# Kernel optimization log

Measured on AMD Instinct MI355X. Metric: run time of the kernel, lower is better.

Reference implementation:

```python
import jax, jax.numpy as jnp
import numpy as np

S, B, K = 1024, 16, 1024
QD, KD = 1024, 1024


def setup_inputs() -> dict:
    key = jax.random.key(0)
    k1, k2, k3, k4 = jax.random.split(key, 4)
    queries = jax.random.normal(k1, (S, B, QD), dtype=jnp.float32)
    keys = jax.random.normal(k2, (B, K, KD), dtype=jnp.float32)
    null_mask = jax.random.randint(k3, (B, K), 0, 2).astype(jnp.bool_)
    W_in = jax.random.normal(k4, (KD, QD), dtype=jnp.float32) * 0.02
    return {"queries": queries, "keys": keys, "null_mask": null_mask, "W_in": W_in}


def reference(queries, keys, null_mask, W_in):
    # queries: (S, B, QD); keys: (B, K, KD); null_mask: (B, K); W_in: (KD, QD)
    t_query = jnp.einsum('sbq,dq->sbd', queries, W_in)          # linear_in, no bias
    alpha = jnp.einsum('sbd,bkd->sbk', t_query, keys)           # unscaled bilinear scores
    alpha = jnp.where(null_mask[None, :, :], -jnp.inf, alpha)   # masked_fill_
    att_weight = jax.nn.softmax(alpha, axis=2)                  # (S, B, K)
    attened_keys = jnp.einsum('sbk,bkd->sbd', att_weight, keys) # (S, B, KD)
    return (attened_keys, alpha)
```

## Files before the change

kernel.cpp:

```cpp
#include <hip/hip_runtime.h>
#include <math.h>

#define S_DIM 1024
#define B_DIM 16
#define K_DIM 1024
#define QD_DIM 1024
#define KD_DIM 1024
#define MASK_NEG (-3.0e38f)

using short8v = __attribute__((ext_vector_type(8))) short;
using float4v = __attribute__((ext_vector_type(4))) float;
using uint4v  = __attribute__((ext_vector_type(4))) uint;

#define MFMA(a, b, c) __builtin_amdgcn_mfma_f32_16x16x32_bf16(a, b, c, 0, 0, 0)
#define BAR()   __builtin_amdgcn_s_barrier()
#define SB0()   __builtin_amdgcn_sched_barrier(0)
#define PRIO(x) __builtin_amdgcn_s_setprio(x)
#define VMCNT(N) asm volatile("s_waitcnt vmcnt(" #N ")" ::: "memory")
#define LGKM0()  asm volatile("s_waitcnt lgkmcnt(0)" ::: "memory")


__device__ __forceinline__ void gll16(const void* g, void* l) {
    __builtin_amdgcn_global_load_lds((const __attribute__((address_space(1))) unsigned int*)g,
                                     (__attribute__((address_space(3))) unsigned int*)l,
                                     16, 0, 0);
}

__device__ __forceinline__ void split4(const float4 v, uint2& hi, uint2& lo) {
    uint ax = __float_as_uint(v.x), ay = __float_as_uint(v.y);
    uint az = __float_as_uint(v.z), aw = __float_as_uint(v.w);
    hi.x = __builtin_amdgcn_perm(ay, ax, 0x07060302u);
    hi.y = __builtin_amdgcn_perm(aw, az, 0x07060302u);
    float rx = v.x - __uint_as_float(ax & 0xFFFF0000u);
    float ry = v.y - __uint_as_float(ay & 0xFFFF0000u);
    float rz = v.z - __uint_as_float(az & 0xFFFF0000u);
    float rw = v.w - __uint_as_float(aw & 0xFFFF0000u);
    lo.x = __builtin_amdgcn_perm(__float_as_uint(ry), __float_as_uint(rx), 0x07060302u);
    lo.y = __builtin_amdgcn_perm(__float_as_uint(rw), __float_as_uint(rz), 0x07060302u);
}

__device__ __forceinline__ int twiddle(int l) {
    int b0 = (l ^ (l >> 2) ^ (l >> 4)) & 1;
    int b1 = ((l >> 1) ^ (l >> 3)) & 1;
    int b2 = ((l >> 2) ^ (l >> 4)) & 1;
    return (l & 0x38) | (b2 << 2) | (b1 << 1) | b0;
}
__device__ __forceinline__ int fragoff(int R, int quad) {
    return (((R << 2) | quad) ^ (R & 7)) << 3;
}

struct Ctx {
    int w, quad, l15, wm, wn, srow, scol;
    int arow, ac, ws0, ws1;
    int offA[4], offB[8];
};

__device__ __forceinline__ Ctx make_ctx(int t) {
    Ctx c;
    const int lane = t & 63;
    c.w = t >> 6; c.quad = lane >> 4; c.l15 = lane & 15;
    c.wm = c.w >> 1; c.wn = c.w & 1;
    const int sl = twiddle(lane);
    c.srow = c.w * 32 + (sl >> 2);
    c.scol = (sl & 3) * 8;
    c.arow = t >> 1; c.ac = t & 1;
    const int c0 = c.ac * 2;
    c.ws0 = ((c.arow << 2) | c0) ^ (c.arow & 7);
    c.ws1 = ((c.arow << 2) | (c0 + 1)) ^ (c.arow & 7);
    #pragma unroll
    for (int mt = 0; mt < 4; ++mt) { int R = c.wm * 64 + mt * 16 + c.l15; c.offA[mt] = fragoff(R, c.quad); }
    #pragma unroll
    for (int nt = 0; nt < 8; ++nt) { int R = c.wn * 128 + nt * 16 + c.l15; c.offB[nt] = fragoff(R, c.quad); }
    return c;
}

__device__ __forceinline__ void stage2(const short* __restrict__ plane, int row0, int k0,
                                       short* tile, const Ctx& c) {
    const short* g0 = plane + (size_t)(row0 + c.srow) * 1024 + k0 + c.scol;
    gll16(g0, tile + c.w * 1024);
    gll16(g0 + (size_t)16 * 1024, tile + c.w * 1024 + 512);
}

__device__ __forceinline__ void mfma8x4(const short8v (&a)[4], const short8v (&bb)[8],
                                        float4v (&acc)[4][8]) {
    #pragma unroll
    for (int nt = 0; nt < 8; ++nt)
        #pragma unroll
        for (int mt = 0; mt < 4; ++mt)
            acc[mt][nt] = MFMA(a[mt], bb[nt], acc[mt][nt]);
}

__device__ __forceinline__ void load4(const float4* __restrict__ P, int kn, float4 (&v)[4]) {
    #pragma unroll
    for (int i = 0; i < 4; ++i) v[i] = P[kn / 4 + i];
}

__device__ __forceinline__ void write_split(const float4 (&va)[4], short* N0, short* N1,
                                            int ws0, int ws1) {
    uint2 h[4], l[4];
    #pragma unroll
    for (int i = 0; i < 4; ++i) split4(va[i], h[i], l[i]);
    uint4v v0, v1;
    v0[0] = h[0].x; v0[1] = h[0].y; v0[2] = h[1].x; v0[3] = h[1].y;
    v1[0] = h[2].x; v1[1] = h[2].y; v1[2] = h[3].x; v1[3] = h[3].y;
    *(uint4v*)(N0 + ws0 * 8) = v0;
    *(uint4v*)(N0 + ws1 * 8) = v1;
    v0[0] = l[0].x; v0[1] = l[0].y; v0[2] = l[1].x; v0[3] = l[1].y;
    v1[0] = l[2].x; v1[1] = l[2].y; v1[2] = l[3].x; v1[3] = l[3].y;
    *(uint4v*)(N1 + ws0 * 8) = v0;
    *(uint4v*)(N1 + ws1 * 8) = v1;
}

__device__ __forceinline__ void writeA_exp(const float4 (&va)[4], float Mv, float Lv,
                                           short* N0, short* N1, int ws0, int ws1) {
    float4 p[4];
    #pragma unroll
    for (int i = 0; i < 4; ++i) {
        p[i].x = __expf(va[i].x - Mv) * Lv;
        p[i].y = __expf(va[i].y - Mv) * Lv;
        p[i].z = __expf(va[i].z - Mv) * Lv;
        p[i].w = __expf(va[i].w - Mv) * Lv;
    }
    write_split(p, N0, N1, ws0, ws1);
}

__global__ __launch_bounds__(256) void k_split(const float* __restrict__ src,
                                               short* __restrict__ h, short* __restrict__ l) {
    const size_t base = ((size_t)blockIdx.x * 256 + threadIdx.x) * 4;
    const float4 v = *(const float4*)(src + base);
    uint2 hh, ll;
    split4(v, hh, ll);
    *(uint2*)(h + base) = hh;
    *(uint2*)(l + base) = ll;
}

__global__ __launch_bounds__(256) void k_transpose(const float* __restrict__ keys,
                                                   short* __restrict__ th, short* __restrict__ tl) {
    __shared__ float T[32][33];
    const int t = threadIdx.x;
    const int b = blockIdx.z, d0 = blockIdx.x * 32, k0 = blockIdx.y * 32;
    const float* Kb = keys + (size_t)b * K_DIM * KD_DIM;
    const int ry = t >> 3, cx = (t & 7) * 4;
    const float4 v = *(const float4*)(Kb + (size_t)(k0 + ry) * KD_DIM + d0 + cx);
    T[ry][cx] = v.x; T[ry][cx + 1] = v.y; T[ry][cx + 2] = v.z; T[ry][cx + 3] = v.w;
    __syncthreads();
    float4 g;
    g.x = T[cx][ry]; g.y = T[cx + 1][ry]; g.z = T[cx + 2][ry]; g.w = T[cx + 3][ry];
    uint2 hh, ll;
    split4(g, hh, ll);
    const size_t o = (size_t)b * K_DIM * KD_DIM + (size_t)(d0 + ry) * K_DIM + k0 + cx;
    *(uint2*)(th + o) = hh;
    *(uint2*)(tl + o) = ll;
}

__global__ __launch_bounds__(256) void k_stats(const float* __restrict__ alpha,
                                               float* __restrict__ mx,
                                               float* __restrict__ il) {
    const int r = blockIdx.x;
    const int t = threadIdx.x;
    const float4 v = ((const float4*)(alpha + (size_t)r * K_DIM))[t];
    float m = fmaxf(fmaxf(v.x, v.y), fmaxf(v.z, v.w));
    #pragma unroll
    for (int o = 1; o < 64; o <<= 1) m = fmaxf(m, __shfl_xor(m, o, 64));
    __shared__ float redm[4];
    __shared__ float reds[4];
    const int wid = t >> 6;
    if ((t & 63) == 0) redm[wid] = m;
    __syncthreads();
    const float M = fmaxf(fmaxf(redm[0], redm[1]), fmaxf(redm[2], redm[3]));
    float s = expf(v.x - M) + expf(v.y - M) + expf(v.z - M) + expf(v.w - M);
    #pragma unroll
    for (int o = 1; o < 64; o <<= 1) s += __shfl_xor(s, o, 64);
    if ((t & 63) == 0) reds[wid] = s;
    __syncthreads();
    if (t == 0) {
        mx[r] = M;
        il[r] = 1.0f / (reds[0] + reds[1] + reds[2] + reds[3]);
    }
}

template<bool DS>
__device__ __forceinline__ void step_g1(const float4* __restrict__ qP, int kn,
                                        const short* __restrict__ Wh, const short* __restrict__ Wl, int n0,
                                        const short* C0, const short* C1, const short* C2, const short* C3,
                                        short* N0, short* N1, short* N2, short* N3,
                                        const Ctx& c, float4v (&acc)[4][8]) {
    short8v ah[4], bh[8];
    #pragma unroll
    for (int mt = 0; mt < 4; ++mt) ah[mt] = *(const short8v*)(C0 + c.offA[mt]);
    #pragma unroll
    for (int nt = 0; nt < 8; ++nt) bh[nt] = *(const short8v*)(C2 + c.offB[nt]);
    float4 qv[4];
    if (DS) { load4(qP, kn, qv); SB0(); stage2(Wh, n0, kn, N2, c); }
    SB0(); BAR(); LGKM0(); SB0();
    PRIO(1); mfma8x4(ah, bh, acc); PRIO(0); SB0(); BAR();

    short8v al[4];
    #pragma unroll
    for (int mt = 0; mt < 4; ++mt) al[mt] = *(const short8v*)(C1 + c.offA[mt]);
    if (DS) { stage2(Wl, n0, kn, N3, c); }
    SB0(); BAR(); LGKM0(); SB0();
    PRIO(1); mfma8x4(al, bh, acc); PRIO(0); SB0(); BAR();

    if (DS) { VMCNT(4); } else { VMCNT(0); }
    SB0(); BAR();
    short8v bl[8];
    #pragma unroll
    for (int nt = 0; nt < 8; ++nt) bl[nt] = *(const short8v*)(C3 + c.offB[nt]);
    LGKM0(); SB0();
    PRIO(1); mfma8x4(ah, bl, acc); PRIO(0);
    if (DS) {
        write_split(qv, N0, N1, c.ws0, c.ws1);
        LGKM0();
        VMCNT(2);
    }
    SB0(); BAR();
}

__global__ __launch_bounds__(512, 2) void g1k(const float* __restrict__ Q,
                                              const short* __restrict__ Wh, const short* __restrict__ Wl,
                                              short* __restrict__ TQh, short* __restrict__ TQl) {
    __shared__ __align__(16) short lds[65536];
    const int t = threadIdx.x;
    const int m0 = blockIdx.y * 256, n0 = blockIdx.x * 256;
    const Ctx c = make_ctx(t);
    const float4* qP = (const float4*)(Q + (size_t)(m0 + c.arow) * QD_DIM + c.ac * 16);
    short *T00 = lds,         *T01 = lds + 8192,  *T02 = lds + 16384, *T03 = lds + 24576;
    short *T10 = lds + 32768, *T11 = lds + 40960, *T12 = lds + 49152, *T13 = lds + 57344;

    float4v acc[4][8] = {};
    {
        float4 qv[4];
        load4(qP, 0, qv); SB0();
        stage2(Wh, n0, 0, T02, c);
        stage2(Wl, n0, 0, T03, c);
        VMCNT(4); SB0();
        write_split(qv, T00, T01, c.ws0, c.ws1);
        LGKM0();
        VMCNT(2); SB0();
        BAR();
    }
    #pragma unroll 1
    for (int it = 0; it < 15; ++it) {
        step_g1<true>(qP, (2 * it + 1) * 32, Wh, Wl, n0, T00, T01, T02, T03, T10, T11, T12, T13, c, acc);
        step_g1<true>(qP, (2 * it + 2) * 32, Wh, Wl, n0, T10, T11, T12, T13, T00, T01, T02, T03, c, acc);
    }
    step_g1<true >(qP, 31 * 32, Wh, Wl, n0, T00, T01, T02, T03, T10, T11, T12, T13, c, acc);
    step_g1<false>(qP, 0,       Wh, Wl, n0, T10, T11, T12, T13, T00, T01, T02, T03, c, acc);

    #pragma unroll
    for (int mt = 0; mt < 4; ++mt)
        #pragma unroll
        for (int reg = 0; reg < 4; ++reg) {
            const int m = m0 + c.wm * 64 + mt * 16 + c.quad * 4 + reg;
            const int s = m >> 4, bq = m & 15;
            short* th = TQh + (size_t)bq * 1048576 + (size_t)s * 1024;
            short* tl = TQl + (size_t)bq * 1048576 + (size_t)s * 1024;
            #pragma unroll
            for (int nt = 0; nt < 8; ++nt) {
                const int n = n0 + c.wn * 128 + nt * 16 + c.l15;
                const float x = acc[mt][nt][reg];
                const uint u = __float_as_uint(x);
                th[n] = (short)(u >> 16);
                const float r2 = x - __uint_as_float(u & 0xFFFF0000u);
                tl[n] = (short)(__float_as_uint(r2) >> 16);
            }
        }
}

template<bool DS>
__device__ __forceinline__ void step_gg(const short* __restrict__ Ahp, const short* __restrict__ Alp,
                                        const short* __restrict__ Bhp, const short* __restrict__ Blp,
                                        int m0, int n0, int kn,
                                        const short* C0, const short* C1, const short* C2, const short* C3,
                                        short* N0, short* N1, short* N2, short* N3,
                                        const Ctx& c, float4v (&acc)[4][8]) {
    short8v ah[4], bh[8];
    #pragma unroll
    for (int mt = 0; mt < 4; ++mt) ah[mt] = *(const short8v*)(C0 + c.offA[mt]);
    #pragma unroll
    for (int nt = 0; nt < 8; ++nt) bh[nt] = *(const short8v*)(C2 + c.offB[nt]);
    if (DS) { stage2(Ahp, m0, kn, N0, c); stage2(Bhp, n0, kn, N2, c); VMCNT(4); }
    else    { VMCNT(0); }
    SB0(); BAR(); LGKM0(); SB0();
    PRIO(1); mfma8x4(ah, bh, acc); PRIO(0); SB0(); BAR();

    short8v al[4];
    #pragma unroll
    for (int mt = 0; mt < 4; ++mt) al[mt] = *(const short8v*)(C1 + c.offA[mt]);
    if (DS) { stage2(Alp, m0, kn, N1, c); stage2(Blp, n0, kn, N3, c); }
    SB0(); BAR(); LGKM0(); SB0();
    PRIO(1); mfma8x4(al, bh, acc); PRIO(0); SB0(); BAR();

    short8v bl[8];
    #pragma unroll
    for (int nt = 0; nt < 8; ++nt) bl[nt] = *(const short8v*)(C3 + c.offB[nt]);
    if (DS) { VMCNT(4); }
    SB0(); BAR(); LGKM0(); SB0();
    PRIO(1); mfma8x4(ah, bl, acc); PRIO(0); SB0(); BAR();
}

__device__ __forceinline__ void core_gg(const short* __restrict__ Ahp, const short* __restrict__ Alp,
                                        const short* __restrict__ Bhp, const short* __restrict__ Blp,
                                        int m0, int n0, short* lds, const Ctx& c, float4v (&acc)[4][8]) {
    short *T00 = lds,         *T01 = lds + 8192,  *T02 = lds + 16384, *T03 = lds + 24576;
    short *T10 = lds + 32768, *T11 = lds + 40960, *T12 = lds + 49152, *T13 = lds + 57344;
    stage2(Ahp, m0, 0, T00, c); stage2(Bhp, n0, 0, T02, c);
    stage2(Alp, m0, 0, T01, c); stage2(Blp, n0, 0, T03, c);
    VMCNT(4); SB0(); BAR();
    #pragma unroll 1
    for (int it = 0; it < 15; ++it) {
        step_gg<true>(Ahp, Alp, Bhp, Blp, m0, n0, (2 * it + 1) * 32, T00, T01, T02, T03, T10, T11, T12, T13, c, acc);
        step_gg<true>(Ahp, Alp, Bhp, Blp, m0, n0, (2 * it + 2) * 32, T10, T11, T12, T13, T00, T01, T02, T03, c, acc);
    }
    step_gg<true >(Ahp, Alp, Bhp, Blp, m0, n0, 31 * 32, T00, T01, T02, T03, T10, T11, T12, T13, c, acc);
    step_gg<false>(Ahp, Alp, Bhp, Blp, m0, n0, 0,       T10, T11, T12, T13, T00, T01, T02, T03, c, acc);
}

__global__ __launch_bounds__(512, 2) void g2k(const short* __restrict__ TQh, const short* __restrict__ TQl,
                                              const short* __restrict__ Kh, const short* __restrict__ Kl,
                                              const int* __restrict__ mask, float* __restrict__ alpha) {
    __shared__ __align__(16) short lds[65536];
    const int t = threadIdx.x;
    const int m0 = blockIdx.y * 256, n0 = blockIdx.x * 256, b = blockIdx.z;
    const Ctx c = make_ctx(t);
    float4v acc[4][8] = {};
    core_gg(TQh + (size_t)b * 1048576, TQl + (size_t)b * 1048576,
            Kh + (size_t)b * 1048576, Kl + (size_t)b * 1048576, m0, n0, lds, c, acc);
    int mk[8];
    #pragma unroll
    for (int nt = 0; nt < 8; ++nt)
        mk[nt] = mask[b * K_DIM + n0 + c.wn * 128 + nt * 16 + c.l15];
    #pragma unroll
    for (int mt = 0; mt < 4; ++mt)
        #pragma unroll
        for (int reg = 0; reg < 4; ++reg) {
            const int m = m0 + c.wm * 64 + mt * 16 + c.quad * 4 + reg;
            #pragma unroll
            for (int nt = 0; nt < 8; ++nt) {
                const int n = n0 + c.wn * 128 + nt * 16 + c.l15;
                alpha[((size_t)m * B_DIM + b) * K_DIM + n] = mk[nt] ? MASK_NEG : acc[mt][nt][reg];
            }
        }
}

template<bool DS>
__device__ __forceinline__ void step_g3(const float4* __restrict__ aP, int kn,
                                        const short* __restrict__ Bhp, const short* __restrict__ Blp, int n0,
                                        const short* C0, const short* C1, const short* C2, const short* C3,
                                        short* N0, short* N1, short* N2, short* N3,
                                        const Ctx& c, float Mv, float Lv,
                                        float4v (&acc)[4][8]) {
    short8v ah[4], bh[8];
    #pragma unroll
    for (int mt = 0; mt < 4; ++mt) ah[mt] = *(const short8v*)(C0 + c.offA[mt]);
    #pragma unroll
    for (int nt = 0; nt < 8; ++nt) bh[nt] = *(const short8v*)(C2 + c.offB[nt]);
    float4 va[4];
    if (DS) {
        #pragma unroll
        for (int i = 0; i < 4; ++i) va[i] = aP[kn / 4 + i];
        stage2(Bhp, n0, kn, N2, c);
    }
    SB0(); BAR(); LGKM0(); SB0();
    PRIO(1); mfma8x4(ah, bh, acc); PRIO(0); SB0(); BAR();

    short8v al[4];
    #pragma unroll
    for (int mt = 0; mt < 4; ++mt) al[mt] = *(const short8v*)(C1 + c.offA[mt]);
    if (DS) { stage2(Blp, n0, kn, N3, c); }
    SB0(); BAR(); LGKM0(); SB0();
    PRIO(1); mfma8x4(al, bh, acc); PRIO(0); SB0(); BAR();

    if (DS) { VMCNT(4); }
    else    { VMCNT(0); }
    SB0(); BAR();
    short8v bl[8];
    #pragma unroll
    for (int nt = 0; nt < 8; ++nt) bl[nt] = *(const short8v*)(C3 + c.offB[nt]);
    LGKM0(); SB0();
    PRIO(1); mfma8x4(ah, bl, acc); PRIO(0);
    if (DS) {
        writeA_exp(va, Mv, Lv, N0, N1, c.ws0, c.ws1);
        LGKM0();
        VMCNT(2);
    }
    SB0(); BAR();
}

__global__ __launch_bounds__(512, 2) void g3k(const float* __restrict__ alpha,
                                              const short* __restrict__ KTh, const short* __restrict__ KTl,
                                              const float* __restrict__ mx, const float* __restrict__ il,
                                              float* __restrict__ outk) {
    __shared__ __align__(16) short lds[65536];
    const int t = threadIdx.x;
    const int m0 = blockIdx.y * 256, n0 = blockIdx.x * 256, b = blockIdx.z;
    const Ctx c = make_ctx(t);
    const short* Bhp = KTh + (size_t)b * 1048576;
    const short* Blp = KTl + (size_t)b * 1048576;
    const float4* aP = (const float4*)(alpha + ((size_t)(m0 + c.arow) * B_DIM + b) * K_DIM + c.ac * 16);
    const float Mv = mx[(size_t)(m0 + c.arow) * B_DIM + b];
    const float Lv = il[(size_t)(m0 + c.arow) * B_DIM + b];
    short *T00 = lds,         *T01 = lds + 8192,  *T02 = lds + 16384, *T03 = lds + 24576;
    short *T10 = lds + 32768, *T11 = lds + 40960, *T12 = lds + 49152, *T13 = lds + 57344;

    float4v acc[4][8] = {};
    {
        float4 va[4];
        #pragma unroll
        for (int i = 0; i < 4; ++i) va[i] = aP[i];
        stage2(Bhp, n0, 0, T02, c);
        stage2(Blp, n0, 0, T03, c);
        VMCNT(4);
        writeA_exp(va, Mv, Lv, T00, T01, c.ws0, c.ws1);
        LGKM0();
        VMCNT(2);
        SB0(); BAR();
    }
    #pragma unroll 1
    for (int it = 0; it < 15; ++it) {
        step_g3<true>(aP, (2 * it + 1) * 32, Bhp, Blp, n0, T00, T01, T02, T03, T10, T11, T12, T13, c, Mv, Lv, acc);
        step_g3<true>(aP, (2 * it + 2) * 32, Bhp, Blp, n0, T10, T11, T12, T13, T00, T01, T02, T03, c, Mv, Lv, acc);
    }
    step_g3<true >(aP, 31 * 32, Bhp, Blp, n0, T00, T01, T02, T03, T10, T11, T12, T13, c, Mv, Lv, acc);
    step_g3<false>(aP, 0,       Bhp, Blp, n0, T10, T11, T12, T13, T00, T01, T02, T03, c, Mv, Lv, acc);

    #pragma unroll
    for (int mt = 0; mt < 4; ++mt)
        #pragma unroll
        for (int reg = 0; reg < 4; ++reg) {
            const int m = m0 + c.wm * 64 + mt * 16 + c.quad * 4 + reg;
            #pragma unroll
            for (int nt = 0; nt < 8; ++nt) {
                const int n = n0 + c.wn * 128 + nt * 16 + c.l15;
                outk[((size_t)m * B_DIM + b) * KD_DIM + n] = acc[mt][nt][reg];
            }
        }
}

extern "C" void kernel_launch(void* const* d_in, const int* in_sizes, int n_in,
                              void* d_out, int out_size, void* d_ws, size_t ws_size,
                              hipStream_t stream) {
    const float* Q    = (const float*)d_in[0];
    const float* keys = (const float*)d_in[1];
    const int*   mask = (const int*)d_in[2];
    const float* W    = (const float*)d_in[3];

    float* out_att   = (float*)d_out;
    float* out_alpha = out_att + (size_t)S_DIM * B_DIM * KD_DIM;

    const size_t STREAM = (size_t)B_DIM * 1048576;

    short* TQh = (short*)d_ws;
    short* TQl = TQh + STREAM;
    short* KTh = (short*)d_ws;
    short* KTl = KTh + STREAM;
    float* mx  = (float*)((char*)d_ws + ((size_t)64 << 20));
    float* il  = mx + S_DIM * B_DIM;

    short* Wh  = (short*)out_alpha;
    short* Wl  = Wh + 1048576;
    short* Khs = (short*)out_att;
    short* Kls = Khs + STREAM;

    dim3 blk(256), blkg(512);

    k_split<<<dim3(1024), blk, 0, stream>>>(W, Wh, Wl);
    k_split<<<dim3(16384), blk, 0, stream>>>(keys, Khs, Kls);

    g1k<<<dim3(KD_DIM / 256, (S_DIM * B_DIM) / 256), blkg, 0, stream>>>(Q, Wh, Wl, TQh, TQl);

    g2k<<<dim3(K_DIM / 256, S_DIM / 256, B_DIM), blkg, 0, stream>>>(TQh, TQl, Khs, Kls, mask, out_alpha);

    k_transpose<<<dim3(32, 32, B_DIM), blk, 0, stream>>>(keys, KTh, KTl);

    k_stats<<<dim3(S_DIM * B_DIM), blk, 0, stream>>>(out_alpha, mx, il);

    g3k<<<dim3(KD_DIM / 256, S_DIM / 256, B_DIM), blkg, 0, stream>>>(out_alpha, KTh, KTl, mx, il, out_att);
}
```

Baseline: 553.2 us.

## Restructure split-bf16 GEMM steps: one barrier per k-step, prefetch next fragments in registers

Rewrites the per-k-step schedule of all three split-bf16 GEMM kernels. Instead of three barrier-separated MFMA phases per step, each step issues all global→LDS stages up front and carries the next step's al/bh fragments in registers across iterations. It then overlaps LDS reads of ah/bl with MFMAs using partial lgkmcnt waits and needs only one block barrier per step. The cost is more live vector registers and a full vmcnt(0) wait each step, which could expose global load latency.

```diff
diff --git a/kernel.cpp b/kernel.cpp
--- a/kernel.cpp
+++ b/kernel.cpp
@@ -17,7 +17,7 @@
 #define SB0()   __builtin_amdgcn_sched_barrier(0)
 #define PRIO(x) __builtin_amdgcn_s_setprio(x)
 #define VMCNT(N) asm volatile("s_waitcnt vmcnt(" #N ")" ::: "memory")
-#define LGKM0()  asm volatile("s_waitcnt lgkmcnt(0)" ::: "memory")
+#define LGKMC(N) asm volatile("s_waitcnt lgkmcnt(" #N ")" ::: "memory")
 
 
 __device__ __forceinline__ void gll16(const void* g, void* l) {
@@ -88,6 +88,15 @@
         #pragma unroll
         for (int mt = 0; mt < 4; ++mt)
             acc[mt][nt] = MFMA(a[mt], bb[nt], acc[mt][nt]);
+}
+
+__device__ __forceinline__ void readA(const short* T, const Ctx& c, short8v (&a)[4]) {
+    #pragma unroll
+    for (int mt = 0; mt < 4; ++mt) a[mt] = *(const short8v*)(T + c.offA[mt]);
+}
+__device__ __forceinline__ void readB(const short* T, const Ctx& c, short8v (&b)[8]) {
+    #pragma unroll
+    for (int nt = 0; nt < 8; ++nt) b[nt] = *(const short8v*)(T + c.offB[nt]);
 }
 
 __device__ __forceinline__ void load4(const float4* __restrict__ P, int kn, float4 (&v)[4]) {
@@ -179,42 +188,95 @@
     }
 }
 
+
 template<bool DS>
-__device__ __forceinline__ void step_g1(const float4* __restrict__ qP, int kn,
-                                        const short* __restrict__ Wh, const short* __restrict__ Wl, int n0,
-                                        const short* C0, const short* C1, const short* C2, const short* C3,
-                                        short* N0, short* N1, short* N2, short* N3,
-                                        const Ctx& c, float4v (&acc)[4][8]) {
-    short8v ah[4], bh[8];
-    #pragma unroll
-    for (int mt = 0; mt < 4; ++mt) ah[mt] = *(const short8v*)(C0 + c.offA[mt]);
-    #pragma unroll
-    for (int nt = 0; nt < 8; ++nt) bh[nt] = *(const short8v*)(C2 + c.offB[nt]);
+__device__ __forceinline__ void step2(const short* __restrict__ Ahp, const short* __restrict__ Alp,
+                                      const short* __restrict__ Bhp, const short* __restrict__ Blp,
+                                      int m0, int n0, int kn,
+                                      const short* C0, const short* C1, const short* C2, const short* C3,
+                                      short* N0, short* N1, short* N2, short* N3,
+                                      const Ctx& c, short8v (&al)[4], short8v (&bh)[8],
+                                      float4v (&acc)[4][8]) {
+    short8v ah[4], bl[8];
+    if (DS) {
+        stage2(Ahp, m0, kn, N0, c); stage2(Alp, m0, kn, N1, c);
+        stage2(Bhp, n0, kn, N2, c); stage2(Blp, n0, kn, N3, c);
+    }
+    SB0();
+    readA(C0, c, ah); SB0();
+    readB(C3, c, bl); SB0();
+    LGKMC(12); SB0();
+    PRIO(1); mfma8x4(al, bh, acc); PRIO(0); SB0();
+    LGKMC(8); SB0();
+    PRIO(1); mfma8x4(ah, bh, acc); PRIO(0); SB0();
+    LGKMC(0); SB0();
+    if (DS) { VMCNT(0); SB0(); }
+    BAR(); SB0();
+    if (DS) { readA(N1, c, al); SB0(); readB(N2, c, bh); SB0(); }
+    PRIO(1); mfma8x4(ah, bl, acc); PRIO(0); SB0();
+}
+
+template<bool DS>
+__device__ __forceinline__ void step1(const float4* __restrict__ qP, int kn,
+                                      const short* __restrict__ Wh, const short* __restrict__ Wl, int n0,
+                                      const short* C0, const short* C1, const short* C2, const short* C3,
+                                      short* N0, short* N1, short* N2, short* N3,
+                                      const Ctx& c, short8v (&al)[4], short8v (&bh)[8],
+                                      float4v (&acc)[4][8]) {
+    short8v ah[4], bl[8];
     float4 qv[4];
-    if (DS) { load4(qP, kn, qv); SB0(); stage2(Wh, n0, kn, N2, c); }
-    SB0(); BAR(); LGKM0(); SB0();
-    PRIO(1); mfma8x4(ah, bh, acc); PRIO(0); SB0(); BAR();
-
-    short8v al[4];
-    #pragma unroll
-    for (int mt = 0; mt < 4; ++mt) al[mt] = *(const short8v*)(C1 + c.offA[mt]);
-    if (DS) { stage2(Wl, n0, kn, N3, c); }
-    SB0(); BAR(); LGKM0(); SB0();
-    PRIO(1); mfma8x4(al, bh, acc); PRIO(0); SB0(); BAR();
-
-    if (DS) { VMCNT(4); } else { VMCNT(0); }
-    SB0(); BAR();
-    short8v bl[8];
-    #pragma unroll
-    for (int nt = 0; nt < 8; ++nt) bl[nt] = *(const short8v*)(C3 + c.offB[nt]);
-    LGKM0(); SB0();
-    PRIO(1); mfma8x4(ah, bl, acc); PRIO(0);
     if (DS) {
+        load4(qP, kn, qv); SB0();
+        stage2(Wh, n0, kn, N2, c); stage2(Wl, n0, kn, N3, c);
+    }
+    SB0();
+    readA(C0, c, ah); SB0();
+    readB(C3, c, bl); SB0();
+    LGKMC(12); SB0();
+    PRIO(1); mfma8x4(al, bh, acc); PRIO(0); SB0();
+    LGKMC(8); SB0();
+    PRIO(1); mfma8x4(ah, bh, acc); PRIO(0); SB0();
+    LGKMC(0); SB0();
+    if (DS) {
+        VMCNT(0); SB0();
         write_split(qv, N0, N1, c.ws0, c.ws1);
-        LGKM0();
-        VMCNT(2);
-    }
-    SB0(); BAR();
+        LGKMC(0); SB0();
+    }
+    BAR(); SB0();
+    if (DS) { readA(N1, c, al); SB0(); readB(N2, c, bh); SB0(); }
+    PRIO(1); mfma8x4(ah, bl, acc); PRIO(0); SB0();
+}
+
+template<bool DS>
+__device__ __forceinline__ void step3(const float4* __restrict__ aP, int kn,
+                                      const short* __restrict__ Bhp, const short* __restrict__ Blp, int n0,
+                                      const short* C0, const short* C1, const short* C2, const short* C3,
+                                      short* N0, short* N1, short* N2, short* N3,
+                                      const Ctx& c, float Mv, float Lv,
+                                      short8v (&al)[4], short8v (&bh)[8],
+                                      float4v (&acc)[4][8]) {
+    short8v ah[4], bl[8];
+    float4 va[4];
+    if (DS) {
+        load4(aP, kn, va); SB0();
+        stage2(Bhp, n0, kn, N2, c); stage2(Blp, n0, kn, N3, c);
+    }
+    SB0();
+    readA(C0, c, ah); SB0();
+    readB(C3, c, bl); SB0();
+    LGKMC(12); SB0();
+    PRIO(1); mfma8x4(al, bh, acc); PRIO(0); SB0();
+    LGKMC(8); SB0();
+    PRIO(1); mfma8x4(ah, bh, acc); PRIO(0); SB0();
+    LGKMC(0); SB0();
+    if (DS) {
+        VMCNT(0); SB0();
+        writeA_exp(va, Mv, Lv, N0, N1, c.ws0, c.ws1);
+        LGKMC(0); SB0();
+    }
+    BAR(); SB0();
+    if (DS) { readA(N1, c, al); SB0(); readB(N2, c, bh); SB0(); }
+    PRIO(1); mfma8x4(ah, bl, acc); PRIO(0); SB0();
 }
 
 __global__ __launch_bounds__(512, 2) void g1k(const float* __restrict__ Q,
@@ -229,24 +291,26 @@
     short *T10 = lds + 32768, *T11 = lds + 40960, *T12 = lds + 49152, *T13 = lds + 57344;
 
     float4v acc[4][8] = {};
+    short8v al[4], bh[8];
     {
         float4 qv[4];
         load4(qP, 0, qv); SB0();
         stage2(Wh, n0, 0, T02, c);
         stage2(Wl, n0, 0, T03, c);
-        VMCNT(4); SB0();
+        VMCNT(0); SB0();
         write_split(qv, T00, T01, c.ws0, c.ws1);
-        LGKM0();
-        VMCNT(2); SB0();
-        BAR();
+        LGKMC(0); SB0();
+        BAR(); SB0();
+        readA(T01, c, al); SB0();
+        readB(T02, c, bh); SB0();
     }
     #pragma unroll 1
     for (int it = 0; it < 15; ++it) {
-        step_g1<true>(qP, (2 * it + 1) * 32, Wh, Wl, n0, T00, T01, T02, T03, T10, T11, T12, T13, c, acc);
-        step_g1<true>(qP, (2 * it + 2) * 32, Wh, Wl, n0, T10, T11, T12, T13, T00, T01, T02, T03, c, acc);
-    }
-    step_g1<true >(qP, 31 * 32, Wh, Wl, n0, T00, T01, T02, T03, T10, T11, T12, T13, c, acc);
-    step_g1<false>(qP, 0,       Wh, Wl, n0, T10, T11, T12, T13, T00, T01, T02, T03, c, acc);
+        step1<true>(qP, (2 * it + 1) * 32, Wh, Wl, n0, T00, T01, T02, T03, T10, T11, T12, T13, c, al, bh, acc);
+        step1<true>(qP, (2 * it + 2) * 32, Wh, Wl, n0, T10, T11, T12, T13, T00, T01, T02, T03, c, al, bh, acc);
+    }
+    step1<true >(qP, 31 * 32, Wh, Wl, n0, T00, T01, T02, T03, T10, T11, T12, T13, c, al, bh, acc);
+    step1<false>(qP, 0,       Wh, Wl, n0, T10, T11, T12, T13, T00, T01, T02, T03, c, al, bh, acc);
 
     #pragma unroll
     for (int mt = 0; mt < 4; ++mt)
@@ -268,55 +332,6 @@
         }
 }
 
-template<bool DS>
-__device__ __forceinline__ void step_gg(const short* __restrict__ Ahp, const short* __restrict__ Alp,
-                                        const short* __restrict__ Bhp, const short* __restrict__ Blp,
-                                        int m0, int n0, int kn,
-                                        const short* C0, const short* C1, const short* C2, const short* C3,
-                                        short* N0, short* N1, short* N2, short* N3,
-                                        const Ctx& c, float4v (&acc)[4][8]) {
-    short8v ah[4], bh[8];
-    #pragma unroll
-    for (int mt = 0; mt < 4; ++mt) ah[mt] = *(const short8v*)(C0 + c.offA[mt]);
-    #pragma unroll
-    for (int nt = 0; nt < 8; ++nt) bh[nt] = *(const short8v*)(C2 + c.offB[nt]);
-    if (DS) { stage2(Ahp, m0, kn, N0, c); stage2(Bhp, n0, kn, N2, c); VMCNT(4); }
-    else    { VMCNT(0); }
-    SB0(); BAR(); LGKM0(); SB0();
-    PRIO(1); mfma8x4(ah, bh, acc); PRIO(0); SB0(); BAR();
-
-    short8v al[4];
-    #pragma unroll
-    for (int mt = 0; mt < 4; ++mt) al[mt] = *(const short8v*)(C1 + c.offA[mt]);
-    if (DS) { stage2(Alp, m0, kn, N1, c); stage2(Blp, n0, kn, N3, c); }
-    SB0(); BAR(); LGKM0(); SB0();
-    PRIO(1); mfma8x4(al, bh, acc); PRIO(0); SB0(); BAR();
-
-    short8v bl[8];
-    #pragma unroll
-    for (int nt = 0; nt < 8; ++nt) bl[nt] = *(const short8v*)(C3 + c.offB[nt]);
-    if (DS) { VMCNT(4); }
-    SB0(); BAR(); LGKM0(); SB0();
-    PRIO(1); mfma8x4(ah, bl, acc); PRIO(0); SB0(); BAR();
-}
-
-__device__ __forceinline__ void core_gg(const short* __restrict__ Ahp, const short* __restrict__ Alp,
-                                        const short* __restrict__ Bhp, const short* __restrict__ Blp,
-                                        int m0, int n0, short* lds, const Ctx& c, float4v (&acc)[4][8]) {
-    short *T00 = lds,         *T01 = lds + 8192,  *T02 = lds + 16384, *T03 = lds + 24576;
-    short *T10 = lds + 32768, *T11 = lds + 40960, *T12 = lds + 49152, *T13 = lds + 57344;
-    stage2(Ahp, m0, 0, T00, c); stage2(Bhp, n0, 0, T02, c);
-    stage2(Alp, m0, 0, T01, c); stage2(Blp, n0, 0, T03, c);
-    VMCNT(4); SB0(); BAR();
-    #pragma unroll 1
-    for (int it = 0; it < 15; ++it) {
-        step_gg<true>(Ahp, Alp, Bhp, Blp, m0, n0, (2 * it + 1) * 32, T00, T01, T02, T03, T10, T11, T12, T13, c, acc);
-        step_gg<true>(Ahp, Alp, Bhp, Blp, m0, n0, (2 * it + 2) * 32, T10, T11, T12, T13, T00, T01, T02, T03, c, acc);
-    }
-    step_gg<true >(Ahp, Alp, Bhp, Blp, m0, n0, 31 * 32, T00, T01, T02, T03, T10, T11, T12, T13, c, acc);
-    step_gg<false>(Ahp, Alp, Bhp, Blp, m0, n0, 0,       T10, T11, T12, T13, T00, T01, T02, T03, c, acc);
-}
-
 __global__ __launch_bounds__(512, 2) void g2k(const short* __restrict__ TQh, const short* __restrict__ TQl,
                                               const short* __restrict__ Kh, const short* __restrict__ Kl,
                                               const int* __restrict__ mask, float* __restrict__ alpha) {
@@ -324,9 +339,31 @@
     const int t = threadIdx.x;
     const int m0 = blockIdx.y * 256, n0 = blockIdx.x * 256, b = blockIdx.z;
     const Ctx c = make_ctx(t);
+    const short* Ahp = TQh + (size_t)b * 1048576;
+    const short* Alp = TQl + (size_t)b * 1048576;
+    const short* Bhp = Kh + (size_t)b * 1048576;
+    const short* Blp = Kl + (size_t)b * 1048576;
+    short *T00 = lds,         *T01 = lds + 8192,  *T02 = lds + 16384, *T03 = lds + 24576;
+    short *T10 = lds + 32768, *T11 = lds + 40960, *T12 = lds + 49152, *T13 = lds + 57344;
+
     float4v acc[4][8] = {};
-    core_gg(TQh + (size_t)b * 1048576, TQl + (size_t)b * 1048576,
-            Kh + (size_t)b * 1048576, Kl + (size_t)b * 1048576, m0, n0, lds, c, acc);
+    short8v al[4], bh[8];
+    {
+        stage2(Ahp, m0, 0, T00, c); stage2(Alp, m0, 0, T01, c);
+        stage2(Bhp, n0, 0, T02, c); stage2(Blp, n0, 0, T03, c);
+        VMCNT(0); SB0();
+        BAR(); SB0();
+        readA(T01, c, al); SB0();
+        readB(T02, c, bh); SB0();
+    }
+    #pragma unroll 1
+    for (int it = 0; it < 15; ++it) {
+        step2<true>(Ahp, Alp, Bhp, Blp, m0, n0, (2 * it + 1) * 32, T00, T01, T02, T03, T10, T11, T12, T13, c, al, bh, acc);
+        step2<true>(Ahp, Alp, Bhp, Blp, m0, n0, (2 * it + 2) * 32, T10, T11, T12, T13, T00, T01, T02, T03, c, al, bh, acc);
+    }
+    step2<true >(Ahp, Alp, Bhp, Blp, m0, n0, 31 * 32, T00, T01, T02, T03, T10, T11, T12, T13, c, al, bh, acc);
+    step2<false>(Ahp, Alp, Bhp, Blp, m0, n0, 0,       T10, T11, T12, T13, T00, T01, T02, T03, c, al, bh, acc);
+
     int mk[8];
     #pragma unroll
     for (int nt = 0; nt < 8; ++nt)
@@ -342,50 +379,6 @@
                 alpha[((size_t)m * B_DIM + b) * K_DIM + n] = mk[nt] ? MASK_NEG : acc[mt][nt][reg];
             }
         }
-}
-
-template<bool DS>
-__device__ __forceinline__ void step_g3(const float4* __restrict__ aP, int kn,
-                                        const short* __restrict__ Bhp, const short* __restrict__ Blp, int n0,
-                                        const short* C0, const short* C1, const short* C2, const short* C3,
-                                        short* N0, short* N1, short* N2, short* N3,
-                                        const Ctx& c, float Mv, float Lv,
-                                        float4v (&acc)[4][8]) {
-    short8v ah[4], bh[8];
-    #pragma unroll
-    for (int mt = 0; mt < 4; ++mt) ah[mt] = *(const short8v*)(C0 + c.offA[mt]);
-    #pragma unroll
-    for (int nt = 0; nt < 8; ++nt) bh[nt] = *(const short8v*)(C2 + c.offB[nt]);
-    float4 va[4];
-    if (DS) {
-        #pragma unroll
-        for (int i = 0; i < 4; ++i) va[i] = aP[kn / 4 + i];
-        stage2(Bhp, n0, kn, N2, c);
-    }
-    SB0(); BAR(); LGKM0(); SB0();
-    PRIO(1); mfma8x4(ah, bh, acc); PRIO(0); SB0(); BAR();
-
-    short8v al[4];
-    #pragma unroll
-    for (int mt = 0; mt < 4; ++mt) al[mt] = *(const short8v*)(C1 + c.offA[mt]);
-    if (DS) { stage2(Blp, n0, kn, N3, c); }
-    SB0(); BAR(); LGKM0(); SB0();
-    PRIO(1); mfma8x4(al, bh, acc); PRIO(0); SB0(); BAR();
-
-    if (DS) { VMCNT(4); }
-    else    { VMCNT(0); }
-    SB0(); BAR();
-    short8v bl[8];
-    #pragma unroll
-    for (int nt = 0; nt < 8; ++nt) bl[nt] = *(const short8v*)(C3 + c.offB[nt]);
-    LGKM0(); SB0();
-    PRIO(1); mfma8x4(ah, bl, acc); PRIO(0);
-    if (DS) {
-        writeA_exp(va, Mv, Lv, N0, N1, c.ws0, c.ws1);
-        LGKM0();
-        VMCNT(2);
-    }
-    SB0(); BAR();
 }
 
 __global__ __launch_bounds__(512, 2) void g3k(const float* __restrict__ alpha,
@@ -405,25 +398,26 @@
     short *T10 = lds + 32768, *T11 = lds + 40960, *T12 = lds + 49152, *T13 = lds + 57344;
 
     float4v acc[4][8] = {};
+    short8v al[4], bh[8];
     {
         float4 va[4];
-        #pragma unroll
-        for (int i = 0; i < 4; ++i) va[i] = aP[i];
+        load4(aP, 0, va); SB0();
         stage2(Bhp, n0, 0, T02, c);
         stage2(Blp, n0, 0, T03, c);
-        VMCNT(4);
+        VMCNT(0); SB0();
         writeA_exp(va, Mv, Lv, T00, T01, c.ws0, c.ws1);
-        LGKM0();
-        VMCNT(2);
-        SB0(); BAR();
+        LGKMC(0); SB0();
+        BAR(); SB0();
+        readA(T01, c, al); SB0();
+        readB(T02, c, bh); SB0();
     }
     #pragma unroll 1
     for (int it = 0; it < 15; ++it) {
-        step_g3<true>(aP, (2 * it + 1) * 32, Bhp, Blp, n0, T00, T01, T02, T03, T10, T11, T12, T13, c, Mv, Lv, acc);
-        step_g3<true>(aP, (2 * it + 2) * 32, Bhp, Blp, n0, T10, T11, T12, T13, T00, T01, T02, T03, c, Mv, Lv, acc);
-    }
-    step_g3<true >(aP, 31 * 32, Bhp, Blp, n0, T00, T01, T02, T03, T10, T11, T12, T13, c, Mv, Lv, acc);
-    step_g3<false>(aP, 0,       Bhp, Blp, n0, T10, T11, T12, T13, T00, T01, T02, T03, c, Mv, Lv, acc);
+        step3<true>(aP, (2 * it + 1) * 32, Bhp, Blp, n0, T00, T01, T02, T03, T10, T11, T12, T13, c, Mv, Lv, al, bh, acc);
+        step3<true>(aP, (2 * it + 2) * 32, Bhp, Blp, n0, T10, T11, T12, T13, T00, T01, T02, T03, c, Mv, Lv, al, bh, acc);
+    }
+    step3<true >(aP, 31 * 32, Bhp, Blp, n0, T00, T01, T02, T03, T10, T11, T12, T13, c, Mv, Lv, al, bh, acc);
+    step3<false>(aP, 0,       Bhp, Blp, n0, T10, T11, T12, T13, T00, T01, T02, T03, c, Mv, Lv, al, bh, acc);
 
     #pragma unroll
     for (int mt = 0; mt < 4; ++mt)
```

Result: slower. 785.3 us (+42.0%).

## Fuse softmax partial max/sum into score GEMM epilogue and merge split launches

Applied to the files above, without the earlier changes.

The score GEMM epilogue now computes per-row partial max and exp-sum over its 256-column tile using shuffles and LDS, and writes them to workspace. A tiny stats kernel then combines the four partials per row. This replaces the full re-read of the 64MB alpha tensor in the old stats kernel. The two split launches are also merged into one kernel. The fusion path runs only if the workspace is large enough, and it adds exp work and barriers to the GEMM epilogue.

```diff
diff --git a/kernel.cpp b/kernel.cpp
--- a/kernel.cpp
+++ b/kernel.cpp
@@ -124,14 +124,26 @@
     write_split(p, N0, N1, ws0, ws1);
 }
 
-__global__ __launch_bounds__(256) void k_split(const float* __restrict__ src,
-                                               short* __restrict__ h, short* __restrict__ l) {
-    const size_t base = ((size_t)blockIdx.x * 256 + threadIdx.x) * 4;
-    const float4 v = *(const float4*)(src + base);
+
+__global__ __launch_bounds__(256) void k_split2(const float* __restrict__ W,
+                                                const float* __restrict__ keys,
+                                                short* __restrict__ Wh, short* __restrict__ Wl,
+                                                short* __restrict__ Kh, short* __restrict__ Kl) {
+    const int bid = blockIdx.x;
     uint2 hh, ll;
-    split4(v, hh, ll);
-    *(uint2*)(h + base) = hh;
-    *(uint2*)(l + base) = ll;
+    if (bid < 1024) {
+        const size_t base = ((size_t)bid * 256 + threadIdx.x) * 4;
+        const float4 v = *(const float4*)(W + base);
+        split4(v, hh, ll);
+        *(uint2*)(Wh + base) = hh;
+        *(uint2*)(Wl + base) = ll;
+    } else {
+        const size_t base = ((size_t)(bid - 1024) * 256 + threadIdx.x) * 4;
+        const float4 v = *(const float4*)(keys + base);
+        split4(v, hh, ll);
+        *(uint2*)(Kh + base) = hh;
+        *(uint2*)(Kl + base) = ll;
+    }
 }
 
 __global__ __launch_bounds__(256) void k_transpose(const float* __restrict__ keys,
@@ -179,6 +191,20 @@
     }
 }
 
+__global__ __launch_bounds__(256) void k_stats2(const float* __restrict__ pm,
+                                                const float* __restrict__ ps,
+                                                float* __restrict__ mx,
+                                                float* __restrict__ il) {
+    const int r = blockIdx.x * 256 + threadIdx.x;
+    const float4 m4 = *(const float4*)(pm + (size_t)r * 4);
+    const float4 s4 = *(const float4*)(ps + (size_t)r * 4);
+    const float M = fmaxf(fmaxf(m4.x, m4.y), fmaxf(m4.z, m4.w));
+    const float S = s4.x * expf(m4.x - M) + s4.y * expf(m4.y - M)
+                  + s4.z * expf(m4.z - M) + s4.w * expf(m4.w - M);
+    mx[r] = M;
+    il[r] = 1.0f / S;
+}
+
 template<bool DS>
 __device__ __forceinline__ void step_g1(const float4* __restrict__ qP, int kn,
                                         const short* __restrict__ Wh, const short* __restrict__ Wl, int n0,
@@ -319,7 +345,9 @@
 
 __global__ __launch_bounds__(512, 2) void g2k(const short* __restrict__ TQh, const short* __restrict__ TQl,
                                               const short* __restrict__ Kh, const short* __restrict__ Kl,
-                                              const int* __restrict__ mask, float* __restrict__ alpha) {
+                                              const int* __restrict__ mask, float* __restrict__ alpha,
+                                              float* __restrict__ pm, float* __restrict__ ps,
+                                              int dofuse) {
     __shared__ __align__(16) short lds[65536];
     const int t = threadIdx.x;
     const int m0 = blockIdx.y * 256, n0 = blockIdx.x * 256, b = blockIdx.z;
@@ -342,6 +370,46 @@
                 alpha[((size_t)m * B_DIM + b) * K_DIM + n] = mk[nt] ? MASK_NEG : acc[mt][nt][reg];
             }
         }
+    if (dofuse) {
+        __syncthreads();
+        float* Pm = (float*)lds;
+        float* Ps = ((float*)lds) + 512;
+        #pragma unroll
+        for (int mt = 0; mt < 4; ++mt)
+            #pragma unroll
+            for (int reg = 0; reg < 4; ++reg) {
+                float mloc = MASK_NEG;
+                #pragma unroll
+                for (int nt = 0; nt < 8; ++nt) {
+                    const float x = mk[nt] ? MASK_NEG : acc[mt][nt][reg];
+                    mloc = fmaxf(mloc, x);
+                }
+                #pragma unroll
+                for (int o = 1; o < 16; o <<= 1) mloc = fmaxf(mloc, __shfl_xor(mloc, o, 64));
+                float sloc = 0.0f;
+                #pragma unroll
+                for (int nt = 0; nt < 8; ++nt) {
+                    const float x = mk[nt] ? MASK_NEG : acc[mt][nt][reg];
+                    sloc += expf(x - mloc);
+                }
+                #pragma unroll
+                for (int o = 1; o < 16; o <<= 1) sloc += __shfl_xor(sloc, o, 64);
+                if (c.l15 == 0) {
+                    const int row = c.wm * 64 + mt * 16 + c.quad * 4 + reg;
+                    Pm[row * 2 + c.wn] = mloc;
+                    Ps[row * 2 + c.wn] = sloc;
+                }
+            }
+        __syncthreads();
+        if (t < 256) {
+            const float ma = Pm[t * 2], mb = Pm[t * 2 + 1];
+            const float M = fmaxf(ma, mb);
+            const float S = Ps[t * 2] * expf(ma - M) + Ps[t * 2 + 1] * expf(mb - M);
+            const size_t r = (size_t)(m0 + t) * B_DIM + b;
+            pm[r * 4 + blockIdx.x] = M;
+            ps[r * 4 + blockIdx.x] = S;
+        }
+    }
 }
 
 template<bool DS>
@@ -457,6 +525,11 @@
     short* KTl = KTh + STREAM;
     float* mx  = (float*)((char*)d_ws + ((size_t)64 << 20));
     float* il  = mx + S_DIM * B_DIM;
+    float* pm  = il + S_DIM * B_DIM;
+    float* ps  = pm + S_DIM * B_DIM * 4;
+
+    const size_t need = ((size_t)64 << 20) + (size_t)640 * 1024;
+    const int dofuse = (ws_size >= need) ? 1 : 0;
 
     short* Wh  = (short*)out_alpha;
     short* Wl  = Wh + 1048576;
@@ -465,16 +538,19 @@
 
     dim3 blk(256), blkg(512);
 
-    k_split<<<dim3(1024), blk, 0, stream>>>(W, Wh, Wl);
-    k_split<<<dim3(16384), blk, 0, stream>>>(keys, Khs, Kls);
+    k_split2<<<dim3(1024 + 16384), blk, 0, stream>>>(W, keys, Wh, Wl, Khs, Kls);
 
     g1k<<<dim3(KD_DIM / 256, (S_DIM * B_DIM) / 256), blkg, 0, stream>>>(Q, Wh, Wl, TQh, TQl);
 
-    g2k<<<dim3(K_DIM / 256, S_DIM / 256, B_DIM), blkg, 0, stream>>>(TQh, TQl, Khs, Kls, mask, out_alpha);
+    g2k<<<dim3(K_DIM / 256, S_DIM / 256, B_DIM), blkg, 0, stream>>>(TQh, TQl, Khs, Kls, mask, out_alpha,
+                                                                    pm, ps, dofuse);
 
     k_transpose<<<dim3(32, 32, B_DIM), blk, 0, stream>>>(keys, KTh, KTl);
 
-    k_stats<<<dim3(S_DIM * B_DIM), blk, 0, stream>>>(out_alpha, mx, il);
+    if (dofuse)
+        k_stats2<<<dim3((S_DIM * B_DIM) / 256), blk, 0, stream>>>(pm, ps, mx, il);
+    else
+        k_stats<<<dim3(S_DIM * B_DIM), blk, 0, stream>>>(out_alpha, mx, il);
 
     g3k<<<dim3(KD_DIM / 256, S_DIM / 256, B_DIM), blkg, 0, stream>>>(out_alpha, KTh, KTl, mx, il, out_att);
 }
```

Measured after the change: 555.5 us. About the same (+0.4%).
